# Performance work log

Measured on AMD Instinct MI355X. Metric: run time of the kernel, lower is better.

The kernel has to match this reference:

```python
import jax, jax.numpy as jnp
import numpy as np

EPS = 1e-6
BIG = 1e10

# ---- exact Euclidean distance transform (same math as the O(HW*Nfg) brute force,
# factored over rows: d^2(p, fg) = min_{r'} [ (y-r')^2 + min_{x': fg[r',x']} (x-x')^2 ] ----
def edt_2d(fg):  # fg: [H, W] bool -> [H, W] float distance to nearest True pixel
    H, W = fg.shape
    x = jnp.arange(W, dtype=jnp.float32)
    col_d2 = (x[:, None] - x[None, :]) ** 2                              # [W(x), W(x')]
    # colmin[r', x] = min over fg columns x' in row r' of (x-x')^2
    colmin = jnp.min(jnp.where(fg[:, None, :], col_d2[None, :, :], BIG), axis=-1)  # [H, W]
    y = jnp.arange(H, dtype=jnp.float32)
    row_d2 = (y[:, None] - y[None, :]) ** 2                              # [H(y), H(r')]
    d2 = jnp.min(colmin[None, :, :] + row_d2[:, :, None], axis=1)        # [H, W]
    max_dist = jnp.sqrt(jnp.asarray((H - 1) ** 2 + (W - 1) ** 2, jnp.float32))
    has_fg = jnp.any(fg)
    d2_safe = jnp.minimum(d2, (max_dist ** 2))  # only hit when fg empty
    return jnp.where(has_fg, jnp.sqrt(d2_safe), max_dist)


def signed_distance_map(gt):  # gt: [B,1,H,W] float in {0,1}
    gt_bool = gt[:, 0] > 0.5                                             # [B,H,W]
    dist_outside = jax.vmap(edt_2d)(gt_bool)
    dist_inside = jax.vmap(edt_2d)(~gt_bool)
    phi = jnp.where(gt_bool, -dist_inside, dist_outside)                 # [B,H,W]
    return phi[:, None]                                                  # [B,1,H,W]


def boundary_loss(s_theta, g):
    phi = signed_distance_map(g)
    weight = jnp.exp(-jnp.abs(phi) / 10.0)
    return jnp.mean(weight * jnp.abs(phi * s_theta))


def bce_loss(p, t):  # torch nn.BCELoss (log clamped at -100)
    logp = jnp.clip(jnp.log(p), -100.0)
    log1mp = jnp.clip(jnp.log(1.0 - p), -100.0)
    return -jnp.mean(t * logp + (1.0 - t) * log1mp)


def focal_loss(pred, target, alpha=0.25, gamma=2.0):
    pred = jnp.clip(pred, EPS, 1.0 - EPS)
    pt = pred * target + (1.0 - pred) * (1.0 - target)
    alpha_t = alpha * target + (1.0 - alpha) * (1.0 - target)
    return jnp.mean(-alpha_t * (1.0 - pt) ** gamma * jnp.log(pt))


def _gaussian_kernel(ksize=11, sigma=1.5):
    c = (ksize - 1) / 2.0
    g = np.exp(-((np.arange(ksize) - c) ** 2) / (2.0 * sigma ** 2))
    g = g / g.sum()
    k = np.outer(g, g).astype(np.float32)
    return jnp.asarray(k)[None, None]  # [1,1,K,K]

_SSIM_K = _gaussian_kernel()


def _gconv(x):  # x: [B,1,H,W], valid gaussian filter
    return jax.lax.conv_general_dilated(x, _SSIM_K, (1, 1), 'VALID',
                                        dimension_numbers=('NCHW', 'OIHW', 'NCHW'))


def ssim(x, y, data_range=1.0):
    C1 = (0.01 * data_range) ** 2
    C2 = (0.03 * data_range) ** 2
    mu_x, mu_y = _gconv(x), _gconv(y)
    sx = _gconv(x * x) - mu_x ** 2
    sy = _gconv(y * y) - mu_y ** 2
    sxy = _gconv(x * y) - mu_x * mu_y
    num = (2 * mu_x * mu_y + C1) * (2 * sxy + C2)
    den = (mu_x ** 2 + mu_y ** 2 + C1) * (sx + sy + C2)
    return jnp.mean(num / den)


DICE_W = 1.0
BOUNDARY_W = 1.0
FOCAL_W = 1.0
MSE_W = 1.0
FOCAL_ALPHA = 0.25
FOCAL_GAMMA = 2.0


def setup_inputs() -> dict:
    key = jax.random.key(0)
    k1, k2 = jax.random.split(key)
    pred_masks = jax.random.normal(k1, (8, 1, 192, 192), dtype=jnp.float32)
    target_masks = jax.random.randint(k2, (8, 1, 192, 192), 0, 2, dtype=jnp.int32)
    return {"pred_masks": pred_masks, "target_masks": target_masks}


def reference(pred_masks, target_masks):
    t = target_masks.astype(jnp.float32)
    p = jax.nn.sigmoid(pred_masks)
    dice_val = bce_loss(p, t) * DICE_W
    boundary_val = boundary_loss(p, t) * BOUNDARY_W
    focal_val = focal_loss(p, t, FOCAL_ALPHA, FOCAL_GAMMA) * FOCAL_W
    mse_val = ssim(p, t, 1.0) * MSE_W
    return dice_val + boundary_val + focal_val + mse_val
```

## Files before the change

kernel.cpp:

```cpp
#include <hip/hip_runtime.h>
#include <math.h>

#define BATCH 8
#define HH 192
#define WW 192
#define BIGF 1e10f
#define NROWBLK (BATCH * HH)
#define OH (HH - 10)
#define OW (WW - 10)
#define NSSIMBLK (BATCH * OH)
#define NENVBLK (BATCH * WW)

__device__ __forceinline__ float waveReduceAdd(float v) {
    #pragma unroll
    for (int o = 32; o > 0; o >>= 1) v += __shfl_down(v, o, 64);
    return v;
}

__device__ __forceinline__ int nearestDist(const unsigned long long m0,
                                           const unsigned long long m1,
                                           const unsigned long long m2,
                                           int x) {
    const unsigned long long m[3] = {m0, m1, m2};
    const int wi = x >> 6, b = x & 63;
    int dL = 1 << 29;
    const unsigned long long low = m[wi] << (63 - b);
    if (low) dL = __clzll(low);
    else if (wi >= 1 && m[wi - 1]) dL = b + 1 + __clzll(m[wi - 1]);
    else if (wi == 2 && m[0]) dL = b + 65 + __clzll(m[0]);
    int dR = 1 << 29;
    const unsigned long long high = m[wi] >> b;
    if (high) dR = __ffsll((long long)high) - 1;
    else if (wi <= 1 && m[wi + 1]) dR = (64 - b) + __ffsll((long long)m[wi + 1]) - 1;
    else if (wi == 0 && m[2]) dR = (128 - b) + __ffsll((long long)m[2]) - 1;
    return min(dL, dR);
}

__global__ void prepKernel(const float* __restrict__ pred,
                           const int* __restrict__ tgt,
                           uint2* __restrict__ colminT,
                           float* __restrict__ ssimPart) {
    __shared__ __align__(16) float smem[5 * WW];
    __shared__ unsigned long long lmask[3];
    const int x = threadIdx.x;

    if (blockIdx.x < NROWBLK) {
        const int b = blockIdx.x / HH, r = blockIdx.x % HH;
        const float z = pred[(b * HH + r) * WW + x];
        const int t = tgt[(b * HH + r) * WW + x];
        const int fg = (t > 0) ? 1 : 0;
        const unsigned long long bal = __ballot(fg);
        if ((x & 63) == 0) lmask[x >> 6] = bal;
        __syncthreads();
        const unsigned long long f0 = lmask[0], f1 = lmask[1], f2 = lmask[2];
        int dfg = nearestDist(f0, f1, f2, x);
        int dbg = nearestDist(~f0, ~f1, ~f2, x);
        dfg = min(dfg, 255);
        dbg = min(dbg, 255);
        colminT[((size_t)b * WW + x) * HH + r] =
            make_uint2(__float_as_uint(z), (unsigned)(dfg | (dbg << 8) | (fg << 16)));
    } else {
        const int blk = blockIdx.x - NROWBLK;
        const int b = blk / OH, yo = blk % OH;

        float g[11];
        {
            float s = 0.0f;
            #pragma unroll
            for (int k = 0; k < 11; ++k) {
                const float d = (float)(k - 5);
                g[k] = __expf(-d * d / 4.5f);
                s += g[k];
            }
            const float inv = 1.0f / s;
            #pragma unroll
            for (int k = 0; k < 11; ++k) g[k] *= inv;
        }

        float* sp = smem;
        float* st = smem + WW;
        float* spp = smem + 2 * WW;
        float* stt = smem + 3 * WW;
        float* spt = smem + 4 * WW;

        float ap = 0, at = 0, app = 0, att = 0, apt = 0;
        #pragma unroll
        for (int k = 0; k < 11; ++k) {
            const int row = yo + k;
            const float z = pred[(b * HH + row) * WW + x];
            const float p = 1.0f / (1.0f + __expf(-z));
            const float t = (float)tgt[(b * HH + row) * WW + x];
            const float gk = g[k];
            ap += gk * p; at += gk * t;
            app += gk * p * p; att += gk * t * t; apt += gk * p * t;
        }
        sp[x] = ap; st[x] = at; spp[x] = app; stt[x] = att; spt[x] = apt;
        __syncthreads();

        float term = 0.0f;
        if (x < OW) {
            float mx = 0, my = 0, mxx = 0, myy = 0, mxy = 0;
            #pragma unroll
            for (int k = 0; k < 11; ++k) {
                mx += g[k] * sp[x + k];  my += g[k] * st[x + k];
                mxx += g[k] * spp[x + k]; myy += g[k] * stt[x + k];
                mxy += g[k] * spt[x + k];
            }
            const float C1 = 1e-4f, C2 = 9e-4f;
            const float sx = mxx - mx * mx, sy = myy - my * my, sxy = mxy - mx * my;
            const float num = (2.0f * mx * my + C1) * (2.0f * sxy + C2);
            const float den = (mx * mx + my * my + C1) * (sx + sy + C2);
            term = num / den;
        }
        __shared__ float red1[3];
        const float s = waveReduceAdd(term);
        const int wid = x >> 6;
        if ((x & 63) == 0) red1[wid] = s;
        __syncthreads();
        if (x == 0) ssimPart[blk] = red1[0] + red1[1] + red1[2];
    }
}

__global__ void envKernel(const uint2* __restrict__ colminT,
                          float4* __restrict__ envPart) {
    const int b = blockIdx.x / WW, cx = blockIdx.x % WW;
    const int y = threadIdx.x;

    __shared__ __align__(16) float2 scf[HH];
    const uint2 v = colminT[((size_t)b * WW + cx) * HH + y];
    const int dfg = v.y & 255, dbg = (v.y >> 8) & 255;
    scf[y] = make_float2(dfg == 255 ? BIGF : (float)(dfg * dfg),
                         dbg == 255 ? BIGF : (float)(dbg * dbg));
    __syncthreads();

    float o0 = BIGF, o1 = BIGF, o2 = BIGF, o3 = BIGF;
    float i0 = BIGF, i1 = BIGF, i2 = BIGF, i3 = BIGF;
    const float fy = (float)y;
    #pragma unroll 6
    for (int rp = 0; rp < HH; rp += 4) {
        const float4 v0 = *(const float4*)&scf[rp];
        const float4 v1 = *(const float4*)&scf[rp + 2];
        const float e0 = fy - (float)rp;
        const float e1 = fy - (float)(rp + 1);
        const float e2 = fy - (float)(rp + 2);
        const float e3 = fy - (float)(rp + 3);
        o0 = fminf(o0, fmaf(e0, e0, v0.x)); i0 = fminf(i0, fmaf(e0, e0, v0.y));
        o1 = fminf(o1, fmaf(e1, e1, v0.z)); i1 = fminf(i1, fmaf(e1, e1, v0.w));
        o2 = fminf(o2, fmaf(e2, e2, v1.x)); i2 = fminf(i2, fmaf(e2, e2, v1.y));
        o3 = fminf(o3, fmaf(e3, e3, v1.z)); i3 = fminf(i3, fmaf(e3, e3, v1.w));
    }
    const float d2o = fminf(fminf(o0, o1), fminf(o2, o3));
    const float d2i = fminf(fminf(i0, i1), fminf(i2, i3));

    const float maxd2 = (float)((HH - 1) * (HH - 1) + (WW - 1) * (WW - 1));
    const float dist_out = sqrtf(fminf(d2o, maxd2));
    const float dist_in  = sqrtf(fminf(d2i, maxd2));

    const float tf = (float)((v.y >> 16) & 255);
    const float phi = (tf > 0.5f) ? -dist_in : dist_out;
    const float z = __uint_as_float(v.x);
    const float p = 1.0f / (1.0f + __expf(-z));

    const float wgt = __expf(-fabsf(phi) * 0.1f);
    const float bnd = wgt * fabsf(phi * p);

    const float logp   = fmaxf(__logf(p), -100.0f);
    const float log1mp = fmaxf(__logf(1.0f - p), -100.0f);
    const float bce = -(tf * logp + (1.0f - tf) * log1mp);

    const float pc = fminf(fmaxf(p, 1e-6f), 1.0f - 1e-6f);
    const float pt = pc * tf + (1.0f - pc) * (1.0f - tf);
    const float at = 0.25f * tf + 0.75f * (1.0f - tf);
    const float om = 1.0f - pt;
    const float focal = -at * om * om * __logf(pt);

    __shared__ float red[3][3];
    const float sb = waveReduceAdd(bce);
    const float sf = waveReduceAdd(focal);
    const float sd = waveReduceAdd(bnd);
    const int wid = y >> 6;
    if ((y & 63) == 0) { red[wid][0] = sb; red[wid][1] = sf; red[wid][2] = sd; }
    __syncthreads();
    if (y == 0) {
        envPart[blockIdx.x] = make_float4(red[0][0] + red[1][0] + red[2][0],
                                          red[0][1] + red[1][1] + red[2][1],
                                          red[0][2] + red[1][2] + red[2][2], 0.0f);
    }
}

__global__ void reduceKernel(const float4* __restrict__ envPart,
                             const float* __restrict__ ssimPart,
                             float* __restrict__ out) {
    const int tid = threadIdx.x;
    float s0 = 0, s1 = 0, s2 = 0, s3 = 0;
    for (int i = tid; i < NENVBLK; i += 1024) {
        const float4 v = envPart[i];
        s0 += v.x; s1 += v.y; s2 += v.z;
    }
    for (int i = tid; i < NSSIMBLK; i += 1024) s3 += ssimPart[i];
    s0 = waveReduceAdd(s0); s1 = waveReduceAdd(s1);
    s2 = waveReduceAdd(s2); s3 = waveReduceAdd(s3);
    __shared__ float red[16][4];
    const int wid = tid >> 6;
    if ((tid & 63) == 0) { red[wid][0] = s0; red[wid][1] = s1; red[wid][2] = s2; red[wid][3] = s3; }
    __syncthreads();
    if (tid == 0) {
        float t0 = 0, t1 = 0, t2 = 0, t3 = 0;
        #pragma unroll
        for (int w = 0; w < 16; ++w) { t0 += red[w][0]; t1 += red[w][1]; t2 += red[w][2]; t3 += red[w][3]; }
        const float N1 = (float)(BATCH * HH * WW);
        const float N2 = (float)(BATCH * OH * OW);
        out[0] = (t0 + t1 + t2) / N1 + t3 / N2;
    }
}

extern "C" void kernel_launch(void* const* d_in, const int* in_sizes, int n_in,
                              void* d_out, int out_size, void* d_ws, size_t ws_size,
                              hipStream_t stream) {
    const float* pred = (const float*)d_in[0];
    const int* tgt = (const int*)d_in[1];

    float4* envPart = (float4*)d_ws;
    float* ssimPart = (float*)((char*)d_ws + 24576);
    uint2* colminT = (uint2*)((char*)d_ws + 65536);

    prepKernel<<<NROWBLK + NSSIMBLK, WW, 0, stream>>>(pred, tgt, colminT, ssimPart);
    envKernel<<<NENVBLK, WW, 0, stream>>>(colminT, envPart);
    reduceKernel<<<1, 1024, 0, stream>>>(envPart, ssimPart, (float*)d_out);
}
```

Baseline: 27.58 us.

## Fuse row-mask prep into EDT column kernel, process three columns per block

Removes the separate prep pass and its transposed intermediate buffer. Each EDT block now reads the whole target image for its batch, builds per-row ballot masks in shared memory, computes row-wise nearest distances for three columns, then runs the column min-plus scan and the loss terms. This saves one kernel launch and a global round trip. In exchange, every block re-reads the full target image (64 blocks per batch), and the per-block work is serialised across 192 rows.

```diff
diff --git a/kernel.cpp b/kernel.cpp
--- a/kernel.cpp
+++ b/kernel.cpp
@@ -5,11 +5,11 @@
 #define HH 192
 #define WW 192
 #define BIGF 1e10f
-#define NROWBLK (BATCH * HH)
 #define OH (HH - 10)
 #define OW (WW - 10)
 #define NSSIMBLK (BATCH * OH)
-#define NENVBLK (BATCH * WW)
+#define COLS_PER_BLK 3
+#define NENVBLK (BATCH * WW / COLS_PER_BLK)
 
 __device__ __forceinline__ float waveReduceAdd(float v) {
     #pragma unroll
@@ -36,32 +36,106 @@
     return min(dL, dR);
 }
 
-__global__ void prepKernel(const float* __restrict__ pred,
+__global__ void mainKernel(const float* __restrict__ pred,
                            const int* __restrict__ tgt,
-                           uint2* __restrict__ colminT,
+                           float4* __restrict__ envPart,
                            float* __restrict__ ssimPart) {
-    __shared__ __align__(16) float smem[5 * WW];
-    __shared__ unsigned long long lmask[3];
     const int x = threadIdx.x;
 
-    if (blockIdx.x < NROWBLK) {
-        const int b = blockIdx.x / HH, r = blockIdx.x % HH;
-        const float z = pred[(b * HH + r) * WW + x];
-        const int t = tgt[(b * HH + r) * WW + x];
-        const int fg = (t > 0) ? 1 : 0;
-        const unsigned long long bal = __ballot(fg);
-        if ((x & 63) == 0) lmask[x >> 6] = bal;
-        __syncthreads();
-        const unsigned long long f0 = lmask[0], f1 = lmask[1], f2 = lmask[2];
-        int dfg = nearestDist(f0, f1, f2, x);
-        int dbg = nearestDist(~f0, ~f1, ~f2, x);
-        dfg = min(dfg, 255);
-        dbg = min(dbg, 255);
-        colminT[((size_t)b * WW + x) * HH + r] =
-            make_uint2(__float_as_uint(z), (unsigned)(dfg | (dbg << 8) | (fg << 16)));
+    if (blockIdx.x < NENVBLK) {
+        const int b = blockIdx.x / (WW / COLS_PER_BLK);
+        const int c0 = (blockIdx.x % (WW / COLS_PER_BLK)) * COLS_PER_BLK;
+
+        __shared__ unsigned long long rowm[3][HH];
+        __shared__ __align__(16) float scf[COLS_PER_BLK][HH];
+        __shared__ __align__(16) float scb[COLS_PER_BLK][HH];
+        __shared__ float red[3][3];
+
+        const int wid = x >> 6;
+        const int lane0 = ((x & 63) == 0);
+        #pragma unroll 4
+        for (int r = 0; r < HH; ++r) {
+            const int t = tgt[(b * HH + r) * WW + x];
+            const unsigned long long bal = __ballot(t > 0);
+            if (lane0) rowm[wid][r] = bal;
+        }
+        __syncthreads();
+
+        const int y = x;
+        const unsigned long long f0 = rowm[0][y], f1 = rowm[1][y], f2 = rowm[2][y];
+        float pz[COLS_PER_BLK];
+        float tfv[COLS_PER_BLK];
+        #pragma unroll
+        for (int cc = 0; cc < COLS_PER_BLK; ++cc) {
+            const int col = c0 + cc;
+            const int dfg = nearestDist(f0, f1, f2, col);
+            const int dbg = nearestDist(~f0, ~f1, ~f2, col);
+            const int dfc = min(dfg, 255), dbc = min(dbg, 255);
+            scf[cc][y] = (dfg >= 192) ? BIGF : (float)(dfc * dfc);
+            scb[cc][y] = (dbg >= 192) ? BIGF : (float)(dbc * dbc);
+            pz[cc] = pred[(b * HH + y) * WW + col];
+            const unsigned long long fw = (col < 64) ? f0 : (col < 128) ? f1 : f2;
+            tfv[cc] = (float)((fw >> (col & 63)) & 1ull);
+        }
+        __syncthreads();
+
+        float bceA = 0.0f, focA = 0.0f, bndA = 0.0f;
+        const float fy = (float)y;
+        const float maxd2 = (float)((HH - 1) * (HH - 1) + (WW - 1) * (WW - 1));
+        #pragma unroll
+        for (int cc = 0; cc < COLS_PER_BLK; ++cc) {
+            float o0 = BIGF, o1 = BIGF, o2 = BIGF, o3 = BIGF;
+            float i0 = BIGF, i1 = BIGF, i2 = BIGF, i3 = BIGF;
+            #pragma unroll 6
+            for (int rp = 0; rp < HH; rp += 4) {
+                const float4 vf = *(const float4*)&scf[cc][rp];
+                const float4 vb = *(const float4*)&scb[cc][rp];
+                const float e0 = fy - (float)rp;
+                const float e1 = fy - (float)(rp + 1);
+                const float e2 = fy - (float)(rp + 2);
+                const float e3 = fy - (float)(rp + 3);
+                o0 = fminf(o0, fmaf(e0, e0, vf.x)); i0 = fminf(i0, fmaf(e0, e0, vb.x));
+                o1 = fminf(o1, fmaf(e1, e1, vf.y)); i1 = fminf(i1, fmaf(e1, e1, vb.y));
+                o2 = fminf(o2, fmaf(e2, e2, vf.z)); i2 = fminf(i2, fmaf(e2, e2, vb.z));
+                o3 = fminf(o3, fmaf(e3, e3, vf.w)); i3 = fminf(i3, fmaf(e3, e3, vb.w));
+            }
+            const float d2o = fminf(fminf(o0, o1), fminf(o2, o3));
+            const float d2i = fminf(fminf(i0, i1), fminf(i2, i3));
+            const float dist_out = sqrtf(fminf(d2o, maxd2));
+            const float dist_in  = sqrtf(fminf(d2i, maxd2));
+
+            const float tf = tfv[cc];
+            const float phi = (tf > 0.5f) ? -dist_in : dist_out;
+            const float p = 1.0f / (1.0f + __expf(-pz[cc]));
+
+            const float wgt = __expf(-fabsf(phi) * 0.1f);
+            bndA += wgt * fabsf(phi * p);
+            const float logp   = fmaxf(__logf(p), -100.0f);
+            const float log1mp = fmaxf(__logf(1.0f - p), -100.0f);
+            bceA += -(tf * logp + (1.0f - tf) * log1mp);
+            const float pc = fminf(fmaxf(p, 1e-6f), 1.0f - 1e-6f);
+            const float pt = pc * tf + (1.0f - pc) * (1.0f - tf);
+            const float at = 0.25f * tf + 0.75f * (1.0f - tf);
+            const float om = 1.0f - pt;
+            focA += -at * om * om * __logf(pt);
+        }
+
+        const float sb = waveReduceAdd(bceA);
+        const float sf = waveReduceAdd(focA);
+        const float sd = waveReduceAdd(bndA);
+        if ((x & 63) == 0) { red[wid][0] = sb; red[wid][1] = sf; red[wid][2] = sd; }
+        __syncthreads();
+        if (x == 0) {
+            envPart[blockIdx.x] = make_float4(red[0][0] + red[1][0] + red[2][0],
+                                              red[0][1] + red[1][1] + red[2][1],
+                                              red[0][2] + red[1][2] + red[2][2], 0.0f);
+        }
     } else {
-        const int blk = blockIdx.x - NROWBLK;
+        const int blk = blockIdx.x - NENVBLK;
         const int b = blk / OH, yo = blk % OH;
+
+        __shared__ __align__(16) float smem[5 * WW];
+        __shared__ float red1[3];
 
         float g[11];
         {
@@ -112,79 +186,11 @@
             const float den = (mx * mx + my * my + C1) * (sx + sy + C2);
             term = num / den;
         }
-        __shared__ float red1[3];
         const float s = waveReduceAdd(term);
         const int wid = x >> 6;
         if ((x & 63) == 0) red1[wid] = s;
         __syncthreads();
         if (x == 0) ssimPart[blk] = red1[0] + red1[1] + red1[2];
-    }
-}
-
-__global__ void envKernel(const uint2* __restrict__ colminT,
-                          float4* __restrict__ envPart) {
-    const int b = blockIdx.x / WW, cx = blockIdx.x % WW;
-    const int y = threadIdx.x;
-
-    __shared__ __align__(16) float2 scf[HH];
-    const uint2 v = colminT[((size_t)b * WW + cx) * HH + y];
-    const int dfg = v.y & 255, dbg = (v.y >> 8) & 255;
-    scf[y] = make_float2(dfg == 255 ? BIGF : (float)(dfg * dfg),
-                         dbg == 255 ? BIGF : (float)(dbg * dbg));
-    __syncthreads();
-
-    float o0 = BIGF, o1 = BIGF, o2 = BIGF, o3 = BIGF;
-    float i0 = BIGF, i1 = BIGF, i2 = BIGF, i3 = BIGF;
-    const float fy = (float)y;
-    #pragma unroll 6
-    for (int rp = 0; rp < HH; rp += 4) {
-        const float4 v0 = *(const float4*)&scf[rp];
-        const float4 v1 = *(const float4*)&scf[rp + 2];
-        const float e0 = fy - (float)rp;
-        const float e1 = fy - (float)(rp + 1);
-        const float e2 = fy - (float)(rp + 2);
-        const float e3 = fy - (float)(rp + 3);
-        o0 = fminf(o0, fmaf(e0, e0, v0.x)); i0 = fminf(i0, fmaf(e0, e0, v0.y));
-        o1 = fminf(o1, fmaf(e1, e1, v0.z)); i1 = fminf(i1, fmaf(e1, e1, v0.w));
-        o2 = fminf(o2, fmaf(e2, e2, v1.x)); i2 = fminf(i2, fmaf(e2, e2, v1.y));
-        o3 = fminf(o3, fmaf(e3, e3, v1.z)); i3 = fminf(i3, fmaf(e3, e3, v1.w));
-    }
-    const float d2o = fminf(fminf(o0, o1), fminf(o2, o3));
-    const float d2i = fminf(fminf(i0, i1), fminf(i2, i3));
-
-    const float maxd2 = (float)((HH - 1) * (HH - 1) + (WW - 1) * (WW - 1));
-    const float dist_out = sqrtf(fminf(d2o, maxd2));
-    const float dist_in  = sqrtf(fminf(d2i, maxd2));
-
-    const float tf = (float)((v.y >> 16) & 255);
-    const float phi = (tf > 0.5f) ? -dist_in : dist_out;
-    const float z = __uint_as_float(v.x);
-    const float p = 1.0f / (1.0f + __expf(-z));
-
-    const float wgt = __expf(-fabsf(phi) * 0.1f);
-    const float bnd = wgt * fabsf(phi * p);
-
-    const float logp   = fmaxf(__logf(p), -100.0f);
-    const float log1mp = fmaxf(__logf(1.0f - p), -100.0f);
-    const float bce = -(tf * logp + (1.0f - tf) * log1mp);
-
-    const float pc = fminf(fmaxf(p, 1e-6f), 1.0f - 1e-6f);
-    const float pt = pc * tf + (1.0f - pc) * (1.0f - tf);
-    const float at = 0.25f * tf + 0.75f * (1.0f - tf);
-    const float om = 1.0f - pt;
-    const float focal = -at * om * om * __logf(pt);
-
-    __shared__ float red[3][3];
-    const float sb = waveReduceAdd(bce);
-    const float sf = waveReduceAdd(focal);
-    const float sd = waveReduceAdd(bnd);
-    const int wid = y >> 6;
-    if ((y & 63) == 0) { red[wid][0] = sb; red[wid][1] = sf; red[wid][2] = sd; }
-    __syncthreads();
-    if (y == 0) {
-        envPart[blockIdx.x] = make_float4(red[0][0] + red[1][0] + red[2][0],
-                                          red[0][1] + red[1][1] + red[2][1],
-                                          red[0][2] + red[1][2] + red[2][2], 0.0f);
     }
 }
 
@@ -221,10 +227,8 @@
     const int* tgt = (const int*)d_in[1];
 
     float4* envPart = (float4*)d_ws;
-    float* ssimPart = (float*)((char*)d_ws + 24576);
-    uint2* colminT = (uint2*)((char*)d_ws + 65536);
-
-    prepKernel<<<NROWBLK + NSSIMBLK, WW, 0, stream>>>(pred, tgt, colminT, ssimPart);
-    envKernel<<<NENVBLK, WW, 0, stream>>>(colminT, envPart);
+    float* ssimPart = (float*)((char*)d_ws + 8192);
+
+    mainKernel<<<NENVBLK + NSSIMBLK, WW, 0, stream>>>(pred, tgt, envPart, ssimPart);
     reduceKernel<<<1, 1024, 0, stream>>>(envPart, ssimPart, (float*)d_out);
 }
```

Result: slower. 44.07 us (+59.8%).

## Move SSIM into env pass, tile SSIM rows, fold final reduce via last-block counter

Applied to the files above, without the earlier changes.

The SSIM computation moves out of the row-EDT prep kernel and into the column-envelope kernel. The final reduction kernel is removed: each block bumps an atomic counter and the last block to finish sums the partials, so there are two launches instead of three. Each SSIM block now produces four output rows from fourteen loaded input rows instead of reloading eleven rows per output row, which cuts redundant loads and sigmoid evaluations. The cost is more registers and shared memory per SSIM block, plus a serial tail in which one block performs the final sum.

```diff
diff --git a/kernel.cpp b/kernel.cpp
--- a/kernel.cpp
+++ b/kernel.cpp
@@ -5,11 +5,14 @@
 #define HH 192
 #define WW 192
 #define BIGF 1e10f
-#define NROWBLK (BATCH * HH)
 #define OH (HH - 10)
 #define OW (WW - 10)
-#define NSSIMBLK (BATCH * OH)
+#define SSIM_ROWS 4
+#define SSIM_BPI ((OH + SSIM_ROWS - 1) / SSIM_ROWS)
+#define NSSIMBLK (BATCH * SSIM_BPI)
 #define NENVBLK (BATCH * WW)
+#define NTOTAL (NSSIMBLK + NENVBLK)
+#define NEDTBLK (BATCH * HH)
 
 __device__ __forceinline__ float waveReduceAdd(float v) {
     #pragma unroll
@@ -36,32 +39,49 @@
     return min(dL, dR);
 }
 
-__global__ void prepKernel(const float* __restrict__ pred,
-                           const int* __restrict__ tgt,
-                           uint2* __restrict__ colminT,
-                           float* __restrict__ ssimPart) {
-    __shared__ __align__(16) float smem[5 * WW];
+__global__ void edtKernel(const float* __restrict__ pred,
+                          const int* __restrict__ tgt,
+                          uint2* __restrict__ colminT,
+                          unsigned* __restrict__ counter) {
     __shared__ unsigned long long lmask[3];
     const int x = threadIdx.x;
-
-    if (blockIdx.x < NROWBLK) {
-        const int b = blockIdx.x / HH, r = blockIdx.x % HH;
-        const float z = pred[(b * HH + r) * WW + x];
-        const int t = tgt[(b * HH + r) * WW + x];
-        const int fg = (t > 0) ? 1 : 0;
-        const unsigned long long bal = __ballot(fg);
-        if ((x & 63) == 0) lmask[x >> 6] = bal;
-        __syncthreads();
-        const unsigned long long f0 = lmask[0], f1 = lmask[1], f2 = lmask[2];
-        int dfg = nearestDist(f0, f1, f2, x);
-        int dbg = nearestDist(~f0, ~f1, ~f2, x);
-        dfg = min(dfg, 255);
-        dbg = min(dbg, 255);
-        colminT[((size_t)b * WW + x) * HH + r] =
-            make_uint2(__float_as_uint(z), (unsigned)(dfg | (dbg << 8) | (fg << 16)));
-    } else {
-        const int blk = blockIdx.x - NROWBLK;
-        const int b = blk / OH, yo = blk % OH;
+    if (blockIdx.x == 0 && x == 0)
+        __hip_atomic_store(counter, 0u, __ATOMIC_RELAXED, __HIP_MEMORY_SCOPE_AGENT);
+    const int b = blockIdx.x / HH, r = blockIdx.x % HH;
+    const float z = pred[(b * HH + r) * WW + x];
+    const int t = tgt[(b * HH + r) * WW + x];
+    const int fg = (t > 0) ? 1 : 0;
+    const unsigned long long bal = __ballot(fg);
+    if ((x & 63) == 0) lmask[x >> 6] = bal;
+    __syncthreads();
+    const unsigned long long f0 = lmask[0], f1 = lmask[1], f2 = lmask[2];
+    int dfg = nearestDist(f0, f1, f2, x);
+    int dbg = nearestDist(~f0, ~f1, ~f2, x);
+    dfg = min(dfg, 255);
+    dbg = min(dbg, 255);
+    colminT[((size_t)b * WW + x) * HH + r] =
+        make_uint2(__float_as_uint(z), (unsigned)(dfg | (dbg << 8) | (fg << 16)));
+}
+
+__global__ void fusedKernel(const float* __restrict__ pred,
+                            const int* __restrict__ tgt,
+                            const uint2* __restrict__ colminT,
+                            float* __restrict__ p0,
+                            float* __restrict__ p1,
+                            float* __restrict__ p2,
+                            float* __restrict__ ssimPart,
+                            unsigned* __restrict__ counter,
+                            float* __restrict__ out) {
+    __shared__ __align__(16) float smem[SSIM_ROWS * 5 * WW];
+    __shared__ float red[3][4];
+    __shared__ int isLastSh;
+    const int x = threadIdx.x;
+    const int wid = x >> 6;
+
+    if (blockIdx.x < NSSIMBLK) {
+        const int blk = blockIdx.x;
+        const int b = blk / SSIM_BPI;
+        const int r0 = (blk % SSIM_BPI) * SSIM_ROWS;
 
         float g[11];
         {
@@ -77,140 +97,164 @@
             for (int k = 0; k < 11; ++k) g[k] *= inv;
         }
 
-        float* sp = smem;
-        float* st = smem + WW;
-        float* spp = smem + 2 * WW;
-        float* stt = smem + 3 * WW;
-        float* spt = smem + 4 * WW;
-
-        float ap = 0, at = 0, app = 0, att = 0, apt = 0;
+        float acc[SSIM_ROWS][5];
         #pragma unroll
-        for (int k = 0; k < 11; ++k) {
-            const int row = yo + k;
-            const float z = pred[(b * HH + row) * WW + x];
-            const float p = 1.0f / (1.0f + __expf(-z));
-            const float t = (float)tgt[(b * HH + row) * WW + x];
-            const float gk = g[k];
-            ap += gk * p; at += gk * t;
-            app += gk * p * p; att += gk * t * t; apt += gk * p * t;
-        }
-        sp[x] = ap; st[x] = at; spp[x] = app; stt[x] = att; spt[x] = apt;
+        for (int o = 0; o < SSIM_ROWS; ++o)
+            #pragma unroll
+            for (int s = 0; s < 5; ++s) acc[o][s] = 0.0f;
+
+        #pragma unroll
+        for (int j = 0; j < SSIM_ROWS + 10; ++j) {
+            const int row = r0 + j;
+            float p = 0.0f, t = 0.0f;
+            if (row < HH) {
+                const float z = pred[(b * HH + row) * WW + x];
+                p = 1.0f / (1.0f + __expf(-z));
+                t = (float)tgt[(b * HH + row) * WW + x];
+            }
+            const float pp = p * p, tt = t * t, pt = p * t;
+            #pragma unroll
+            for (int o = 0; o < SSIM_ROWS; ++o) {
+                const int k = j - o;
+                if (k >= 0 && k <= 10) {
+                    const float gk = g[k];
+                    acc[o][0] += gk * p;  acc[o][1] += gk * t;
+                    acc[o][2] += gk * pp; acc[o][3] += gk * tt; acc[o][4] += gk * pt;
+                }
+            }
+        }
+        #pragma unroll
+        for (int o = 0; o < SSIM_ROWS; ++o)
+            #pragma unroll
+            for (int s = 0; s < 5; ++s) smem[(o * 5 + s) * WW + x] = acc[o][s];
         __syncthreads();
 
         float term = 0.0f;
         if (x < OW) {
-            float mx = 0, my = 0, mxx = 0, myy = 0, mxy = 0;
-            #pragma unroll
-            for (int k = 0; k < 11; ++k) {
-                mx += g[k] * sp[x + k];  my += g[k] * st[x + k];
-                mxx += g[k] * spp[x + k]; myy += g[k] * stt[x + k];
-                mxy += g[k] * spt[x + k];
-            }
-            const float C1 = 1e-4f, C2 = 9e-4f;
-            const float sx = mxx - mx * mx, sy = myy - my * my, sxy = mxy - mx * my;
-            const float num = (2.0f * mx * my + C1) * (2.0f * sxy + C2);
-            const float den = (mx * mx + my * my + C1) * (sx + sy + C2);
-            term = num / den;
-        }
-        __shared__ float red1[3];
+            #pragma unroll
+            for (int o = 0; o < SSIM_ROWS; ++o) {
+                if (r0 + o < OH) {
+                    float mx = 0, my = 0, mxx = 0, myy = 0, mxy = 0;
+                    #pragma unroll
+                    for (int k = 0; k < 11; ++k) {
+                        mx  += g[k] * smem[(o * 5 + 0) * WW + x + k];
+                        my  += g[k] * smem[(o * 5 + 1) * WW + x + k];
+                        mxx += g[k] * smem[(o * 5 + 2) * WW + x + k];
+                        myy += g[k] * smem[(o * 5 + 3) * WW + x + k];
+                        mxy += g[k] * smem[(o * 5 + 4) * WW + x + k];
+                    }
+                    const float C1 = 1e-4f, C2 = 9e-4f;
+                    const float sx = mxx - mx * mx, sy = myy - my * my, sxy = mxy - mx * my;
+                    const float num = (2.0f * mx * my + C1) * (2.0f * sxy + C2);
+                    const float den = (mx * mx + my * my + C1) * (sx + sy + C2);
+                    term += num / den;
+                }
+            }
+        }
         const float s = waveReduceAdd(term);
-        const int wid = x >> 6;
-        if ((x & 63) == 0) red1[wid] = s;
-        __syncthreads();
-        if (x == 0) ssimPart[blk] = red1[0] + red1[1] + red1[2];
+        if ((x & 63) == 0) red[wid][0] = s;
+        __syncthreads();
+        if (x == 0)
+            __hip_atomic_store(&ssimPart[blk], red[0][0] + red[1][0] + red[2][0],
+                               __ATOMIC_RELAXED, __HIP_MEMORY_SCOPE_AGENT);
+    } else {
+        const int ebid = blockIdx.x - NSSIMBLK;
+        const int b = ebid / WW, cx = ebid % WW;
+        const int y = x;
+
+        float2* scfb = (float2*)smem;
+        const uint2 v = colminT[((size_t)b * WW + cx) * HH + y];
+        const int dfg = v.y & 255, dbg = (v.y >> 8) & 255;
+        scfb[y] = make_float2(dfg == 255 ? BIGF : (float)(dfg * dfg),
+                              dbg == 255 ? BIGF : (float)(dbg * dbg));
+        __syncthreads();
+
+        float o0 = BIGF, o1 = BIGF, o2 = BIGF, o3 = BIGF;
+        float i0 = BIGF, i1 = BIGF, i2 = BIGF, i3 = BIGF;
+        const float fy = (float)y;
+        #pragma unroll 6
+        for (int rp = 0; rp < HH; rp += 4) {
+            const float4 v0 = *(const float4*)&scfb[rp];
+            const float4 v1 = *(const float4*)&scfb[rp + 2];
+            const float e0 = fy - (float)rp;
+            const float e1 = fy - (float)(rp + 1);
+            const float e2 = fy - (float)(rp + 2);
+            const float e3 = fy - (float)(rp + 3);
+            o0 = fminf(o0, fmaf(e0, e0, v0.x)); i0 = fminf(i0, fmaf(e0, e0, v0.y));
+            o1 = fminf(o1, fmaf(e1, e1, v0.z)); i1 = fminf(i1, fmaf(e1, e1, v0.w));
+            o2 = fminf(o2, fmaf(e2, e2, v1.x)); i2 = fminf(i2, fmaf(e2, e2, v1.y));
+            o3 = fminf(o3, fmaf(e3, e3, v1.z)); i3 = fminf(i3, fmaf(e3, e3, v1.w));
+        }
+        const float d2o = fminf(fminf(o0, o1), fminf(o2, o3));
+        const float d2i = fminf(fminf(i0, i1), fminf(i2, i3));
+
+        const float maxd2 = (float)((HH - 1) * (HH - 1) + (WW - 1) * (WW - 1));
+        const float dist_out = sqrtf(fminf(d2o, maxd2));
+        const float dist_in  = sqrtf(fminf(d2i, maxd2));
+
+        const float tf = (float)((v.y >> 16) & 255);
+        const float phi = (tf > 0.5f) ? -dist_in : dist_out;
+        const float z = __uint_as_float(v.x);
+        const float p = 1.0f / (1.0f + __expf(-z));
+
+        const float wgt = __expf(-fabsf(phi) * 0.1f);
+        const float bnd = wgt * fabsf(phi * p);
+
+        const float logp   = fmaxf(__logf(p), -100.0f);
+        const float log1mp = fmaxf(__logf(1.0f - p), -100.0f);
+        const float bce = -(tf * logp + (1.0f - tf) * log1mp);
+
+        const float pc = fminf(fmaxf(p, 1e-6f), 1.0f - 1e-6f);
+        const float pt = pc * tf + (1.0f - pc) * (1.0f - tf);
+        const float at = 0.25f * tf + 0.75f * (1.0f - tf);
+        const float om = 1.0f - pt;
+        const float focal = -at * om * om * __logf(pt);
+
+        const float sb = waveReduceAdd(bce);
+        const float sf = waveReduceAdd(focal);
+        const float sd = waveReduceAdd(bnd);
+        if ((x & 63) == 0) { red[wid][0] = sb; red[wid][1] = sf; red[wid][2] = sd; }
+        __syncthreads();
+        if (x == 0) {
+            __hip_atomic_store(&p0[ebid], red[0][0] + red[1][0] + red[2][0],
+                               __ATOMIC_RELAXED, __HIP_MEMORY_SCOPE_AGENT);
+            __hip_atomic_store(&p1[ebid], red[0][1] + red[1][1] + red[2][1],
+                               __ATOMIC_RELAXED, __HIP_MEMORY_SCOPE_AGENT);
+            __hip_atomic_store(&p2[ebid], red[0][2] + red[1][2] + red[2][2],
+                               __ATOMIC_RELAXED, __HIP_MEMORY_SCOPE_AGENT);
+        }
     }
-}
-
-__global__ void envKernel(const uint2* __restrict__ colminT,
-                          float4* __restrict__ envPart) {
-    const int b = blockIdx.x / WW, cx = blockIdx.x % WW;
-    const int y = threadIdx.x;
-
-    __shared__ __align__(16) float2 scf[HH];
-    const uint2 v = colminT[((size_t)b * WW + cx) * HH + y];
-    const int dfg = v.y & 255, dbg = (v.y >> 8) & 255;
-    scf[y] = make_float2(dfg == 255 ? BIGF : (float)(dfg * dfg),
-                         dbg == 255 ? BIGF : (float)(dbg * dbg));
+
+    if (x == 0) {
+        asm volatile("s_waitcnt vmcnt(0)" ::: "memory");
+        const unsigned old = __hip_atomic_fetch_add(counter, 1u, __ATOMIC_RELAXED,
+                                                    __HIP_MEMORY_SCOPE_AGENT);
+        isLastSh = (old == NTOTAL - 1) ? 1 : 0;
+    }
     __syncthreads();
 
-    float o0 = BIGF, o1 = BIGF, o2 = BIGF, o3 = BIGF;
-    float i0 = BIGF, i1 = BIGF, i2 = BIGF, i3 = BIGF;
-    const float fy = (float)y;
-    #pragma unroll 6
-    for (int rp = 0; rp < HH; rp += 4) {
-        const float4 v0 = *(const float4*)&scf[rp];
-        const float4 v1 = *(const float4*)&scf[rp + 2];
-        const float e0 = fy - (float)rp;
-        const float e1 = fy - (float)(rp + 1);
-        const float e2 = fy - (float)(rp + 2);
-        const float e3 = fy - (float)(rp + 3);
-        o0 = fminf(o0, fmaf(e0, e0, v0.x)); i0 = fminf(i0, fmaf(e0, e0, v0.y));
-        o1 = fminf(o1, fmaf(e1, e1, v0.z)); i1 = fminf(i1, fmaf(e1, e1, v0.w));
-        o2 = fminf(o2, fmaf(e2, e2, v1.x)); i2 = fminf(i2, fmaf(e2, e2, v1.y));
-        o3 = fminf(o3, fmaf(e3, e3, v1.z)); i3 = fminf(i3, fmaf(e3, e3, v1.w));
-    }
-    const float d2o = fminf(fminf(o0, o1), fminf(o2, o3));
-    const float d2i = fminf(fminf(i0, i1), fminf(i2, i3));
-
-    const float maxd2 = (float)((HH - 1) * (HH - 1) + (WW - 1) * (WW - 1));
-    const float dist_out = sqrtf(fminf(d2o, maxd2));
-    const float dist_in  = sqrtf(fminf(d2i, maxd2));
-
-    const float tf = (float)((v.y >> 16) & 255);
-    const float phi = (tf > 0.5f) ? -dist_in : dist_out;
-    const float z = __uint_as_float(v.x);
-    const float p = 1.0f / (1.0f + __expf(-z));
-
-    const float wgt = __expf(-fabsf(phi) * 0.1f);
-    const float bnd = wgt * fabsf(phi * p);
-
-    const float logp   = fmaxf(__logf(p), -100.0f);
-    const float log1mp = fmaxf(__logf(1.0f - p), -100.0f);
-    const float bce = -(tf * logp + (1.0f - tf) * log1mp);
-
-    const float pc = fminf(fmaxf(p, 1e-6f), 1.0f - 1e-6f);
-    const float pt = pc * tf + (1.0f - pc) * (1.0f - tf);
-    const float at = 0.25f * tf + 0.75f * (1.0f - tf);
-    const float om = 1.0f - pt;
-    const float focal = -at * om * om * __logf(pt);
-
-    __shared__ float red[3][3];
-    const float sb = waveReduceAdd(bce);
-    const float sf = waveReduceAdd(focal);
-    const float sd = waveReduceAdd(bnd);
-    const int wid = y >> 6;
-    if ((y & 63) == 0) { red[wid][0] = sb; red[wid][1] = sf; red[wid][2] = sd; }
-    __syncthreads();
-    if (y == 0) {
-        envPart[blockIdx.x] = make_float4(red[0][0] + red[1][0] + red[2][0],
-                                          red[0][1] + red[1][1] + red[2][1],
-                                          red[0][2] + red[1][2] + red[2][2], 0.0f);
-    }
-}
-
-__global__ void reduceKernel(const float4* __restrict__ envPart,
-                             const float* __restrict__ ssimPart,
-                             float* __restrict__ out) {
-    const int tid = threadIdx.x;
-    float s0 = 0, s1 = 0, s2 = 0, s3 = 0;
-    for (int i = tid; i < NENVBLK; i += 1024) {
-        const float4 v = envPart[i];
-        s0 += v.x; s1 += v.y; s2 += v.z;
-    }
-    for (int i = tid; i < NSSIMBLK; i += 1024) s3 += ssimPart[i];
-    s0 = waveReduceAdd(s0); s1 = waveReduceAdd(s1);
-    s2 = waveReduceAdd(s2); s3 = waveReduceAdd(s3);
-    __shared__ float red[16][4];
-    const int wid = tid >> 6;
-    if ((tid & 63) == 0) { red[wid][0] = s0; red[wid][1] = s1; red[wid][2] = s2; red[wid][3] = s3; }
-    __syncthreads();
-    if (tid == 0) {
-        float t0 = 0, t1 = 0, t2 = 0, t3 = 0;
-        #pragma unroll
-        for (int w = 0; w < 16; ++w) { t0 += red[w][0]; t1 += red[w][1]; t2 += red[w][2]; t3 += red[w][3]; }
-        const float N1 = (float)(BATCH * HH * WW);
-        const float N2 = (float)(BATCH * OH * OW);
-        out[0] = (t0 + t1 + t2) / N1 + t3 / N2;
+    if (isLastSh) {
+        float s0 = 0, s1 = 0, s2 = 0, s3 = 0;
+        for (int i = x; i < NENVBLK; i += WW) {
+            s0 += __hip_atomic_load(&p0[i], __ATOMIC_RELAXED, __HIP_MEMORY_SCOPE_AGENT);
+            s1 += __hip_atomic_load(&p1[i], __ATOMIC_RELAXED, __HIP_MEMORY_SCOPE_AGENT);
+            s2 += __hip_atomic_load(&p2[i], __ATOMIC_RELAXED, __HIP_MEMORY_SCOPE_AGENT);
+        }
+        for (int i = x; i < NSSIMBLK; i += WW)
+            s3 += __hip_atomic_load(&ssimPart[i], __ATOMIC_RELAXED, __HIP_MEMORY_SCOPE_AGENT);
+        s0 = waveReduceAdd(s0); s1 = waveReduceAdd(s1);
+        s2 = waveReduceAdd(s2); s3 = waveReduceAdd(s3);
+        __syncthreads();
+        if ((x & 63) == 0) { red[wid][0] = s0; red[wid][1] = s1; red[wid][2] = s2; red[wid][3] = s3; }
+        __syncthreads();
+        if (x == 0) {
+            float t0 = 0, t1 = 0, t2 = 0, t3 = 0;
+            #pragma unroll
+            for (int w = 0; w < 3; ++w) { t0 += red[w][0]; t1 += red[w][1]; t2 += red[w][2]; t3 += red[w][3]; }
+            const float N1 = (float)(BATCH * HH * WW);
+            const float N2 = (float)(BATCH * OH * OW);
+            out[0] = (t0 + t1 + t2) / N1 + t3 / N2;
+        }
     }
 }
 
@@ -220,11 +264,14 @@
     const float* pred = (const float*)d_in[0];
     const int* tgt = (const int*)d_in[1];
 
-    float4* envPart = (float4*)d_ws;
-    float* ssimPart = (float*)((char*)d_ws + 24576);
-    uint2* colminT = (uint2*)((char*)d_ws + 65536);
-
-    prepKernel<<<NROWBLK + NSSIMBLK, WW, 0, stream>>>(pred, tgt, colminT, ssimPart);
-    envKernel<<<NENVBLK, WW, 0, stream>>>(colminT, envPart);
-    reduceKernel<<<1, 1024, 0, stream>>>(envPart, ssimPart, (float*)d_out);
-}
+    unsigned* counter = (unsigned*)d_ws;
+    float* p0 = (float*)((char*)d_ws + 64);
+    float* p1 = p0 + NENVBLK;
+    float* p2 = p1 + NENVBLK;
+    float* ssimPart = p2 + NENVBLK;
+    uint2* colminT = (uint2*)((char*)d_ws + 32768);
+
+    edtKernel<<<NEDTBLK, WW, 0, stream>>>(pred, tgt, colminT, counter);
+    fusedKernel<<<NTOTAL, WW, 0, stream>>>(pred, tgt, colminT, p0, p1, p2,
+                                           ssimPart, counter, (float*)d_out);
+}
```

Measured after the change: 42.13 us. 52.7% more time.

## Move SSIM into loss kernel and replace final reduce with atomics

Applied to the files above, without the earlier changes.

Moves the SSIM blocks from the first kernel into the second kernel, so the envelope and SSIM work share one launch. Each block now adds its scaled partial sum straight into the output with an atomicAdd, which removes the separate single-block reduction kernel and one launch. The output is zeroed by the first kernel. Atomic accumulation makes the float summation order nondeterministic, and the SSIM work now runs after the EDT rows instead of beside them.

```diff
diff --git a/kernel.cpp b/kernel.cpp
--- a/kernel.cpp
+++ b/kernel.cpp
@@ -5,11 +5,11 @@
 #define HH 192
 #define WW 192
 #define BIGF 1e10f
-#define NROWBLK (BATCH * HH)
 #define OH (HH - 10)
 #define OW (WW - 10)
+#define NEDTBLK (BATCH * HH)
+#define NENVBLK (BATCH * WW)
 #define NSSIMBLK (BATCH * OH)
-#define NENVBLK (BATCH * WW)
 
 __device__ __forceinline__ float waveReduceAdd(float v) {
     #pragma unroll
@@ -36,31 +36,97 @@
     return min(dL, dR);
 }
 
-__global__ void prepKernel(const float* __restrict__ pred,
-                           const int* __restrict__ tgt,
-                           uint2* __restrict__ colminT,
-                           float* __restrict__ ssimPart) {
-    __shared__ __align__(16) float smem[5 * WW];
+__global__ void edtKernel(const float* __restrict__ pred,
+                          const int* __restrict__ tgt,
+                          uint2* __restrict__ colminT,
+                          float* __restrict__ out) {
     __shared__ unsigned long long lmask[3];
     const int x = threadIdx.x;
-
-    if (blockIdx.x < NROWBLK) {
-        const int b = blockIdx.x / HH, r = blockIdx.x % HH;
-        const float z = pred[(b * HH + r) * WW + x];
-        const int t = tgt[(b * HH + r) * WW + x];
-        const int fg = (t > 0) ? 1 : 0;
-        const unsigned long long bal = __ballot(fg);
-        if ((x & 63) == 0) lmask[x >> 6] = bal;
-        __syncthreads();
-        const unsigned long long f0 = lmask[0], f1 = lmask[1], f2 = lmask[2];
-        int dfg = nearestDist(f0, f1, f2, x);
-        int dbg = nearestDist(~f0, ~f1, ~f2, x);
-        dfg = min(dfg, 255);
-        dbg = min(dbg, 255);
-        colminT[((size_t)b * WW + x) * HH + r] =
-            make_uint2(__float_as_uint(z), (unsigned)(dfg | (dbg << 8) | (fg << 16)));
+    if (blockIdx.x == 0 && x == 0) out[0] = 0.0f;
+    const int b = blockIdx.x / HH, r = blockIdx.x % HH;
+    const float z = pred[(b * HH + r) * WW + x];
+    const int t = tgt[(b * HH + r) * WW + x];
+    const int fg = (t > 0) ? 1 : 0;
+    const unsigned long long bal = __ballot(fg);
+    if ((x & 63) == 0) lmask[x >> 6] = bal;
+    __syncthreads();
+    const unsigned long long f0 = lmask[0], f1 = lmask[1], f2 = lmask[2];
+    int dfg = nearestDist(f0, f1, f2, x);
+    int dbg = nearestDist(~f0, ~f1, ~f2, x);
+    dfg = min(dfg, 255);
+    dbg = min(dbg, 255);
+    colminT[((size_t)b * WW + x) * HH + r] =
+        make_uint2(__float_as_uint(z), (unsigned)(dfg | (dbg << 8) | (fg << 16)));
+}
+
+__global__ void lossKernel(const float* __restrict__ pred,
+                           const int* __restrict__ tgt,
+                           const uint2* __restrict__ colminT,
+                           float* __restrict__ out) {
+    __shared__ __align__(16) float smem[5 * WW];
+    __shared__ float red[3];
+    const int x = threadIdx.x;
+    const int wid = x >> 6;
+
+    if (blockIdx.x < NENVBLK) {
+        const int b = blockIdx.x / WW, cx = blockIdx.x % WW;
+        const int y = x;
+
+        float2* scfb = (float2*)smem;
+        const uint2 v = colminT[((size_t)b * WW + cx) * HH + y];
+        const int dfg = v.y & 255, dbg = (v.y >> 8) & 255;
+        scfb[y] = make_float2(dfg == 255 ? BIGF : (float)(dfg * dfg),
+                              dbg == 255 ? BIGF : (float)(dbg * dbg));
+        __syncthreads();
+
+        float o0 = BIGF, o1 = BIGF, o2 = BIGF, o3 = BIGF;
+        float i0 = BIGF, i1 = BIGF, i2 = BIGF, i3 = BIGF;
+        const float fy = (float)y;
+        #pragma unroll 6
+        for (int rp = 0; rp < HH; rp += 4) {
+            const float4 v0 = *(const float4*)&scfb[rp];
+            const float4 v1 = *(const float4*)&scfb[rp + 2];
+            const float e0 = fy - (float)rp;
+            const float e1 = fy - (float)(rp + 1);
+            const float e2 = fy - (float)(rp + 2);
+            const float e3 = fy - (float)(rp + 3);
+            o0 = fminf(o0, fmaf(e0, e0, v0.x)); i0 = fminf(i0, fmaf(e0, e0, v0.y));
+            o1 = fminf(o1, fmaf(e1, e1, v0.z)); i1 = fminf(i1, fmaf(e1, e1, v0.w));
+            o2 = fminf(o2, fmaf(e2, e2, v1.x)); i2 = fminf(i2, fmaf(e2, e2, v1.y));
+            o3 = fminf(o3, fmaf(e3, e3, v1.z)); i3 = fminf(i3, fmaf(e3, e3, v1.w));
+        }
+        const float d2o = fminf(fminf(o0, o1), fminf(o2, o3));
+        const float d2i = fminf(fminf(i0, i1), fminf(i2, i3));
+
+        const float maxd2 = (float)((HH - 1) * (HH - 1) + (WW - 1) * (WW - 1));
+        const float dist_out = sqrtf(fminf(d2o, maxd2));
+        const float dist_in  = sqrtf(fminf(d2i, maxd2));
+
+        const float tf = (float)((v.y >> 16) & 255);
+        const float phi = (tf > 0.5f) ? -dist_in : dist_out;
+        const float z = __uint_as_float(v.x);
+        const float p = 1.0f / (1.0f + __expf(-z));
+
+        const float wgt = __expf(-fabsf(phi) * 0.1f);
+        const float bnd = wgt * fabsf(phi * p);
+        const float logp   = fmaxf(__logf(p), -100.0f);
+        const float log1mp = fmaxf(__logf(1.0f - p), -100.0f);
+        const float bce = -(tf * logp + (1.0f - tf) * log1mp);
+        const float pc = fminf(fmaxf(p, 1e-6f), 1.0f - 1e-6f);
+        const float pt = pc * tf + (1.0f - pc) * (1.0f - tf);
+        const float at = 0.25f * tf + 0.75f * (1.0f - tf);
+        const float om = 1.0f - pt;
+        const float focal = -at * om * om * __logf(pt);
+
+        const float s = waveReduceAdd(bce + focal + bnd);
+        if ((x & 63) == 0) red[wid] = s;
+        __syncthreads();
+        if (x == 0) {
+            const float N1 = (float)(BATCH * HH * WW);
+            atomicAdd(out, (red[0] + red[1] + red[2]) * (1.0f / N1));
+        }
     } else {
-        const int blk = blockIdx.x - NROWBLK;
+        const int blk = blockIdx.x - NENVBLK;
         const int b = blk / OH, yo = blk % OH;
 
         float g[11];
@@ -112,105 +178,13 @@
             const float den = (mx * mx + my * my + C1) * (sx + sy + C2);
             term = num / den;
         }
-        __shared__ float red1[3];
         const float s = waveReduceAdd(term);
-        const int wid = x >> 6;
-        if ((x & 63) == 0) red1[wid] = s;
-        __syncthreads();
-        if (x == 0) ssimPart[blk] = red1[0] + red1[1] + red1[2];
-    }
-}
-
-__global__ void envKernel(const uint2* __restrict__ colminT,
-                          float4* __restrict__ envPart) {
-    const int b = blockIdx.x / WW, cx = blockIdx.x % WW;
-    const int y = threadIdx.x;
-
-    __shared__ __align__(16) float2 scf[HH];
-    const uint2 v = colminT[((size_t)b * WW + cx) * HH + y];
-    const int dfg = v.y & 255, dbg = (v.y >> 8) & 255;
-    scf[y] = make_float2(dfg == 255 ? BIGF : (float)(dfg * dfg),
-                         dbg == 255 ? BIGF : (float)(dbg * dbg));
-    __syncthreads();
-
-    float o0 = BIGF, o1 = BIGF, o2 = BIGF, o3 = BIGF;
-    float i0 = BIGF, i1 = BIGF, i2 = BIGF, i3 = BIGF;
-    const float fy = (float)y;
-    #pragma unroll 6
-    for (int rp = 0; rp < HH; rp += 4) {
-        const float4 v0 = *(const float4*)&scf[rp];
-        const float4 v1 = *(const float4*)&scf[rp + 2];
-        const float e0 = fy - (float)rp;
-        const float e1 = fy - (float)(rp + 1);
-        const float e2 = fy - (float)(rp + 2);
-        const float e3 = fy - (float)(rp + 3);
-        o0 = fminf(o0, fmaf(e0, e0, v0.x)); i0 = fminf(i0, fmaf(e0, e0, v0.y));
-        o1 = fminf(o1, fmaf(e1, e1, v0.z)); i1 = fminf(i1, fmaf(e1, e1, v0.w));
-        o2 = fminf(o2, fmaf(e2, e2, v1.x)); i2 = fminf(i2, fmaf(e2, e2, v1.y));
-        o3 = fminf(o3, fmaf(e3, e3, v1.z)); i3 = fminf(i3, fmaf(e3, e3, v1.w));
-    }
-    const float d2o = fminf(fminf(o0, o1), fminf(o2, o3));
-    const float d2i = fminf(fminf(i0, i1), fminf(i2, i3));
-
-    const float maxd2 = (float)((HH - 1) * (HH - 1) + (WW - 1) * (WW - 1));
-    const float dist_out = sqrtf(fminf(d2o, maxd2));
-    const float dist_in  = sqrtf(fminf(d2i, maxd2));
-
-    const float tf = (float)((v.y >> 16) & 255);
-    const float phi = (tf > 0.5f) ? -dist_in : dist_out;
-    const float z = __uint_as_float(v.x);
-    const float p = 1.0f / (1.0f + __expf(-z));
-
-    const float wgt = __expf(-fabsf(phi) * 0.1f);
-    const float bnd = wgt * fabsf(phi * p);
-
-    const float logp   = fmaxf(__logf(p), -100.0f);
-    const float log1mp = fmaxf(__logf(1.0f - p), -100.0f);
-    const float bce = -(tf * logp + (1.0f - tf) * log1mp);
-
-    const float pc = fminf(fmaxf(p, 1e-6f), 1.0f - 1e-6f);
-    const float pt = pc * tf + (1.0f - pc) * (1.0f - tf);
-    const float at = 0.25f * tf + 0.75f * (1.0f - tf);
-    const float om = 1.0f - pt;
-    const float focal = -at * om * om * __logf(pt);
-
-    __shared__ float red[3][3];
-    const float sb = waveReduceAdd(bce);
-    const float sf = waveReduceAdd(focal);
-    const float sd = waveReduceAdd(bnd);
-    const int wid = y >> 6;
-    if ((y & 63) == 0) { red[wid][0] = sb; red[wid][1] = sf; red[wid][2] = sd; }
-    __syncthreads();
-    if (y == 0) {
-        envPart[blockIdx.x] = make_float4(red[0][0] + red[1][0] + red[2][0],
-                                          red[0][1] + red[1][1] + red[2][1],
-                                          red[0][2] + red[1][2] + red[2][2], 0.0f);
-    }
-}
-
-__global__ void reduceKernel(const float4* __restrict__ envPart,
-                             const float* __restrict__ ssimPart,
-                             float* __restrict__ out) {
-    const int tid = threadIdx.x;
-    float s0 = 0, s1 = 0, s2 = 0, s3 = 0;
-    for (int i = tid; i < NENVBLK; i += 1024) {
-        const float4 v = envPart[i];
-        s0 += v.x; s1 += v.y; s2 += v.z;
-    }
-    for (int i = tid; i < NSSIMBLK; i += 1024) s3 += ssimPart[i];
-    s0 = waveReduceAdd(s0); s1 = waveReduceAdd(s1);
-    s2 = waveReduceAdd(s2); s3 = waveReduceAdd(s3);
-    __shared__ float red[16][4];
-    const int wid = tid >> 6;
-    if ((tid & 63) == 0) { red[wid][0] = s0; red[wid][1] = s1; red[wid][2] = s2; red[wid][3] = s3; }
-    __syncthreads();
-    if (tid == 0) {
-        float t0 = 0, t1 = 0, t2 = 0, t3 = 0;
-        #pragma unroll
-        for (int w = 0; w < 16; ++w) { t0 += red[w][0]; t1 += red[w][1]; t2 += red[w][2]; t3 += red[w][3]; }
-        const float N1 = (float)(BATCH * HH * WW);
-        const float N2 = (float)(BATCH * OH * OW);
-        out[0] = (t0 + t1 + t2) / N1 + t3 / N2;
+        if ((x & 63) == 0) red[wid] = s;
+        __syncthreads();
+        if (x == 0) {
+            const float N2 = (float)(BATCH * OH * OW);
+            atomicAdd(out, (red[0] + red[1] + red[2]) * (1.0f / N2));
+        }
     }
 }
 
@@ -220,11 +194,9 @@
     const float* pred = (const float*)d_in[0];
     const int* tgt = (const int*)d_in[1];
 
-    float4* envPart = (float4*)d_ws;
-    float* ssimPart = (float*)((char*)d_ws + 24576);
-    uint2* colminT = (uint2*)((char*)d_ws + 65536);
-
-    prepKernel<<<NROWBLK + NSSIMBLK, WW, 0, stream>>>(pred, tgt, colminT, ssimPart);
-    envKernel<<<NENVBLK, WW, 0, stream>>>(colminT, envPart);
-    reduceKernel<<<1, 1024, 0, stream>>>(envPart, ssimPart, (float*)d_out);
-}
+    uint2* colminT = (uint2*)d_ws;
+    float* out = (float*)d_out;
+
+    edtKernel<<<NEDTBLK, WW, 0, stream>>>(pred, tgt, colminT, out);
+    lossKernel<<<NENVBLK + NSSIMBLK, WW, 0, stream>>>(pred, tgt, colminT, out);
+}
```

New measurement: 54.92 us. +99.1%, slower.
